# Optimization experiments

Hardware: AMD Instinct MI355X
Metric: run time of the kernel (lower is better)

Reference implementation:

```python
import jax, jax.numpy as jnp
import numpy as np

B, S, H, E = 4, 2048, 1024, 8

def setup_inputs() -> dict:
    key = jax.random.key(0)
    k1, k2, k3 = jax.random.split(key, 3)
    scale_g = 1.0 / np.sqrt(H)
    scale_e = 1.0 / np.sqrt(H)
    return {
        "x": jax.random.normal(k1, (B, S, H), dtype=jnp.float32),
        "gate_w": jax.random.normal(k2, (H, E), dtype=jnp.float32) * scale_g,
        "gate_b": jnp.zeros((E,), dtype=jnp.float32),
        "expert_w": jax.random.normal(k3, (E, H, H), dtype=jnp.float32) * scale_e,
        "expert_b": jnp.zeros((E, H), dtype=jnp.float32),
    }

def reference(x, gate_w, gate_b, expert_w, expert_b):
    b, s, h = x.shape
    tok = x.reshape(-1, h)                                  # [T, H]
    # gate: softmax over experts per token
    w = jax.nn.softmax(tok @ gate_w + gate_b, axis=-1)      # [T, E]
    # all experts applied to all tokens (dense MoE)
    eo = jnp.einsum("th,ehd->ted", tok, expert_w) + expert_b[None]  # [T, E, H]
    out = jnp.einsum("te,ted->td", w, eo)                   # [T, H]
    return out.reshape(b, s, h)
```

## Files before the change

kernel.cpp:

```cpp
#include <hip/hip_runtime.h>
#include <stdint.h>

typedef unsigned short u16;
typedef short bf8 __attribute__((ext_vector_type(8)));
typedef float f4 __attribute__((ext_vector_type(4)));

#define TTOK 8192
#define HD   1024
#define NE   8

static __device__ __forceinline__ u16 f2bf(float f) {
  union { float f; uint32_t u; } v; v.f = f;
  return (u16)((v.u + 0x7fffu + ((v.u >> 16) & 1u)) >> 16);
}

__global__ __launch_bounds__(256) void gate_conv_kernel(
    const float* __restrict__ x, const float* __restrict__ gw,
    const float* __restrict__ gb, float* __restrict__ wout,
    u16* __restrict__ abf)
{
  const int t    = blockIdx.x * 4 + (threadIdx.x >> 6);
  const int lane = threadIdx.x & 63;
  const float* xr = x + (size_t)t * HD;
  float p[NE];
#pragma unroll
  for (int e = 0; e < NE; ++e) p[e] = 0.f;
#pragma unroll 4
  for (int h = lane; h < HD; h += 64) {
    const float xv = xr[h];
    abf[(size_t)t * HD + h] = f2bf(xv);
    const float* g = gw + (size_t)h * NE;
#pragma unroll
    for (int e = 0; e < NE; ++e) p[e] += xv * g[e];
  }
#pragma unroll
  for (int e = 0; e < NE; ++e) {
#pragma unroll
    for (int off = 32; off > 0; off >>= 1)
      p[e] += __shfl_xor(p[e], off, 64);
    p[e] += gb[e];
  }
  float m = p[0];
#pragma unroll
  for (int e = 1; e < NE; ++e) m = fmaxf(m, p[e]);
  float s = 0.f;
#pragma unroll
  for (int e = 0; e < NE; ++e) { p[e] = expf(p[e] - m); s += p[e]; }
  const float inv = 1.f / s;
  if (lane == 0) {
#pragma unroll
    for (int e = 0; e < NE; ++e) wout[t * NE + e] = p[e] * inv;
  }
}

__global__ __launch_bounds__(256) void wconv_kernel(
    const float* __restrict__ ew, u16* __restrict__ wt)
{
  __shared__ u16 tile[64][66];
  const int e  = blockIdx.z;
  const int h0 = blockIdx.y * 64;
  const int d0 = blockIdx.x * 64;
  const int c  = threadIdx.x & 63;
  const int r0 = threadIdx.x >> 6;
  const float* src = ew + (size_t)e * HD * HD;
  u16* dst = wt + (size_t)e * HD * HD;
#pragma unroll
  for (int i = 0; i < 16; ++i) {
    const int r = i * 4 + r0;
    tile[r][c] = f2bf(src[(size_t)(h0 + r) * HD + d0 + c]);
  }
  __syncthreads();
#pragma unroll
  for (int i = 0; i < 16; ++i) {
    const int r = i * 4 + r0;
    dst[(size_t)(d0 + r) * HD + h0 + c] = tile[c][r];
  }
}

#define BM 128
#define BN 128
#define BK 64

#define MM(a_, b_, c_) __builtin_amdgcn_mfma_f32_16x16x32_bf16((a_), (b_), (c_), 0, 0, 0)

#define LDFA(off_, m_, kk_) (*(const bf8*)((const char*)As + (off_) + \
    (size_t)(wrb + (m_) * 16 + l15) * 128 + ((((kk_) * 4 + lhi) ^ (l15 & 7)) << 4)))
#define LDFB(off_, n_, kk_) (*(const bf8*)((const char*)Bs + (off_) + \
    (size_t)(wcb + (n_) * 16 + l15) * 128 + ((((kk_) * 4 + lhi) ^ (l15 & 7)) << 4)))

#define GL(srcp_, dstp_) __builtin_amdgcn_global_load_lds( \
    (const __attribute__((address_space(1))) void*)(srcp_), \
    (__attribute__((address_space(3))) void*)(dstp_), 16, 0, 0)

#define STAGE_A(sq_)                                                \
  {                                                                 \
    const int sk_ = ((sq_) & 15) << 6;                              \
    const u16* as_ = aSrc0 + sk_;                                   \
    char* ad_ = (char*)As + stO + tid * 16;                         \
    GL(as_,          ad_);                                          \
    GL(as_ + 32768,  ad_ +  4096);                                  \
    GL(as_ + 65536,  ad_ +  8192);                                  \
    GL(as_ + 98304,  ad_ + 12288);                                  \
  }
#define STAGE_B(sq_)                                                \
  {                                                                 \
    const int se_ = (sq_) >> 4;                                     \
    const int sk_ = ((sq_) & 15) << 6;                              \
    const u16* bs_ = bSrc0 + (size_t)se_ * (HD * HD) + sk_;         \
    char* bd_ = (char*)Bs + stO + tid * 16;                         \
    GL(bs_,          bd_);                                          \
    GL(bs_ + 32768,  bd_ +  4096);                                  \
    GL(bs_ + 65536,  bd_ +  8192);                                  \
    GL(bs_ + 98304,  bd_ + 12288);                                  \
  }

#define MFMA16                                            \
    acc[0][0] = MM(a0, b0, acc[0][0]);                    \
    acc[1][0] = MM(a1, b0, acc[1][0]);                    \
    acc[2][0] = MM(a2, b0, acc[2][0]);                    \
    acc[3][0] = MM(a3, b0, acc[3][0]);                    \
    acc[0][1] = MM(a0, b1, acc[0][1]);                    \
    acc[1][1] = MM(a1, b1, acc[1][1]);                    \
    acc[2][1] = MM(a2, b1, acc[2][1]);                    \
    acc[3][1] = MM(a3, b1, acc[3][1]);                    \
    acc[0][2] = MM(a0, b2, acc[0][2]);                    \
    acc[1][2] = MM(a1, b2, acc[1][2]);                    \
    acc[2][2] = MM(a2, b2, acc[2][2]);                    \
    acc[3][2] = MM(a3, b2, acc[3][2]);                    \
    acc[0][3] = MM(a0, b3, acc[0][3]);                    \
    acc[1][3] = MM(a1, b3, acc[1][3]);                    \
    acc[2][3] = MM(a2, b3, acc[2][3]);                    \
    acc[3][3] = MM(a3, b3, acc[3][3]);

#define READS(kk_)                                        \
    bf8 a0 = LDFA(curO, 0, kk_);                          \
    bf8 a1 = LDFA(curO, 1, kk_);                          \
    bf8 a2 = LDFA(curO, 2, kk_);                          \
    bf8 a3 = LDFA(curO, 3, kk_);                          \
    bf8 b0 = LDFB(curO, 0, kk_);                          \
    bf8 b1 = LDFB(curO, 1, kk_);                          \
    bf8 b2 = LDFB(curO, 2, kk_);                          \
    bf8 b3 = LDFB(curO, 3, kk_);

#define FOLD(e_)                                                      \
  {                                                                   \
    _Pragma("unroll")                                                 \
    for (int mi = 0; mi < 4; ++mi) {                                  \
      const int r_ = wrb + mi * 16 + lhi * 4;                         \
      const float w0 = wgs[(r_ + 0) * 9 + (e_)];                      \
      const float w1 = wgs[(r_ + 1) * 9 + (e_)];                      \
      const float w2 = wgs[(r_ + 2) * 9 + (e_)];                      \
      const float w3 = wgs[(r_ + 3) * 9 + (e_)];                      \
      _Pragma("unroll")                                               \
      for (int ni = 0; ni < 4; ++ni) {                                \
        accO[mi][ni][0] += w0 * acc[mi][ni][0];                       \
        accO[mi][ni][1] += w1 * acc[mi][ni][1];                       \
        accO[mi][ni][2] += w2 * acc[mi][ni][2];                       \
        accO[mi][ni][3] += w3 * acc[mi][ni][3];                       \
        acc[mi][ni] = fz;                                             \
      }                                                               \
    }                                                                 \
  }

#define BAR       __builtin_amdgcn_s_barrier();
#define LGKM0     asm volatile("s_waitcnt lgkmcnt(0)" ::: "memory");
#define VM0       asm volatile("s_waitcnt vmcnt(0)" ::: "memory");
#define PRIO1     __builtin_amdgcn_s_setprio(1);
#define PRIO0     __builtin_amdgcn_s_setprio(0);

__global__ __launch_bounds__(256, 2) void moe_gemm_kernel(
    const u16* __restrict__ A,
    const u16* __restrict__ Wt,
    const float* __restrict__ wg,
    const float* __restrict__ eb,
    float* __restrict__ out)
{
  __shared__ u16 As[2 * BM * BK];
  __shared__ u16 Bs[2 * BN * BK];
  __shared__ float wgs[BM * 9];

  const int bid   = blockIdx.x;
  const int xcd   = bid & 7;
  const int local = bid >> 3;
  const int bm    = xcd * 8 + (local & 7);
  const int bn    = local >> 3;
  const int row0  = bm * BM;
  const int col0  = bn * BN;

  const int tid  = threadIdx.x;
  const int lane = tid & 63;
  const int wid  = tid >> 6;
  const int wr   = wid >> 1;
  const int wc   = wid & 1;
  const int l15  = lane & 15;
  const int lhi  = lane >> 4;
  const int wrb  = wr * 64;
  const int wcb  = wc * 64;

  const int row_in = tid >> 3;
  const int gsw    = (tid & 7) ^ (row_in & 7);
  const u16* aSrc0 = A  + (size_t)(row0 + row_in) * HD + gsw * 8;
  const u16* bSrc0 = Wt + (size_t)(col0 + row_in) * HD + gsw * 8;

  {
    const f4 v = *(const f4*)(wg + (size_t)row0 * NE + tid * 4);
    const int i0 = tid * 4;
#pragma unroll
    for (int j = 0; j < 4; ++j) {
      const int idx = i0 + j;
      wgs[(idx >> 3) * 9 + (idx & 7)] = v[j];
    }
  }
  LGKM0

  const f4 fz = {0.f, 0.f, 0.f, 0.f};
  f4 acc[4][4], accO[4][4];
#pragma unroll
  for (int i = 0; i < 4; ++i)
#pragma unroll
    for (int j = 0; j < 4; ++j) { acc[i][j] = fz; accO[i][j] = fz; }

  int curO = 0, stO = 16384;

  { const int svO = stO; stO = 0; STAGE_A(0) STAGE_B(0) stO = svO; }

  for (int q = 0; q < 127; ++q) {
    VM0
    BAR
    {
      READS(0)
      STAGE_A(q + 1)
      BAR LGKM0 PRIO1
      MFMA16
      PRIO0 BAR
    }
    {
      READS(1)
      STAGE_B(q + 1)
      BAR LGKM0 PRIO1
      MFMA16
      PRIO0
    }
    { const int t_ = curO; curO = stO; stO = t_; }
    if ((q & 15) == 15) FOLD(q >> 4)
  }
  VM0
  BAR
  { READS(0) BAR LGKM0 PRIO1 MFMA16 PRIO0 BAR }
  { READS(1) BAR LGKM0 PRIO1 MFMA16 PRIO0 }
  FOLD(7)

  float ebv[4][8];
#pragma unroll
  for (int ni = 0; ni < 4; ++ni) {
    const int d = col0 + wcb + ni * 16 + l15;
#pragma unroll
    for (int e2 = 0; e2 < NE; ++e2) ebv[ni][e2] = eb[(size_t)e2 * HD + d];
  }
#pragma unroll
  for (int mi = 0; mi < 4; ++mi) {
    const int r_ = wrb + mi * 16 + lhi * 4;
#pragma unroll
    for (int j = 0; j < 4; ++j) {
      const int t = row0 + r_ + j;
      const float* wrow = &wgs[(r_ + j) * 9];
#pragma unroll
      for (int ni = 0; ni < 4; ++ni) {
        const float bias =
            wrow[0] * ebv[ni][0] + wrow[1] * ebv[ni][1] +
            wrow[2] * ebv[ni][2] + wrow[3] * ebv[ni][3] +
            wrow[4] * ebv[ni][4] + wrow[5] * ebv[ni][5] +
            wrow[6] * ebv[ni][6] + wrow[7] * ebv[ni][7];
        const int d = col0 + wcb + ni * 16 + l15;
        out[(size_t)t * HD + d] = accO[mi][ni][j] + bias;
      }
    }
  }
}

extern "C" void kernel_launch(void* const* d_in, const int* in_sizes, int n_in,
                              void* d_out, int out_size, void* d_ws, size_t ws_size,
                              hipStream_t stream) {
  const float* x  = (const float*)d_in[0];
  const float* gw = (const float*)d_in[1];
  const float* gb = (const float*)d_in[2];
  const float* ew = (const float*)d_in[3];
  const float* eb = (const float*)d_in[4];
  float* out = (float*)d_out;

  char* ws = (char*)d_ws;
  u16*   abf   = (u16*)ws;
  u16*   wt    = (u16*)(ws + (size_t)16 * 1024 * 1024);
  float* wgate = (float*)(ws + (size_t)32 * 1024 * 1024);

  gate_conv_kernel<<<dim3(TTOK / 4), dim3(256), 0, stream>>>(x, gw, gb, wgate, abf);
  wconv_kernel<<<dim3(16, 16, 8), dim3(256), 0, stream>>>(ew, wt);
  moe_gemm_kernel<<<dim3((TTOK / BM) * (HD / BN)), dim3(256), 0, stream>>>(abf, wt, wgate, eb, out);
}
```

Measured before the change: 164.4 us.

## Fold gate weights into A tile, split experts across blocks, add combine pass

Scales each A row by its gate weight while staging it into LDS, so the per-expert FOLD step goes away and one accumulator set covers all experts in a block. The grid becomes 256 blocks of 512 threads with 256x256 tiles, and each block handles half of the experts. The second half writes a bf16 partial that a new combine kernel adds into the output. In exchange it adds register-path A loads with conversion work, an extra kernel launch and extra global traffic, and rounds the partial to bf16, which costs precision.

```diff
diff --git a/kernel.cpp b/kernel.cpp
--- a/kernel.cpp
+++ b/kernel.cpp
@@ -4,6 +4,8 @@
 typedef unsigned short u16;
 typedef short bf8 __attribute__((ext_vector_type(8)));
 typedef float f4 __attribute__((ext_vector_type(4)));
+typedef unsigned int u32x4 __attribute__((ext_vector_type(4)));
+typedef short s8v __attribute__((ext_vector_type(8)));
 
 #define TTOK 8192
 #define HD   1024
@@ -12,6 +14,16 @@
 static __device__ __forceinline__ u16 f2bf(float f) {
   union { float f; uint32_t u; } v; v.f = f;
   return (u16)((v.u + 0x7fffu + ((v.u >> 16) & 1u)) >> 16);
+}
+
+static __device__ __forceinline__ uint32_t scale2bf(uint32_t v, float w) {
+  union { float f; uint32_t u; } lo, hi;
+  lo.u = v << 16;
+  hi.u = v & 0xffff0000u;
+  lo.f *= w; hi.f *= w;
+  const uint32_t lr = (lo.u + 0x7fffu + ((lo.u >> 16) & 1u)) >> 16;
+  const uint32_t hr = (hi.u + 0x7fffu + ((hi.u >> 16) & 1u)) & 0xffff0000u;
+  return lr | hr;
 }
 
 __global__ __launch_bounds__(256) void gate_conv_kernel(
@@ -77,8 +89,8 @@
   }
 }
 
-#define BM 128
-#define BN 128
+#define BM 256
+#define BN 256
 #define BK 64
 
 #define MM(a_, b_, c_) __builtin_amdgcn_mfma_f32_16x16x32_bf16((a_), (b_), (c_), 0, 0, 0)
@@ -92,190 +104,260 @@
     (const __attribute__((address_space(1))) void*)(srcp_), \
     (__attribute__((address_space(3))) void*)(dstp_), 16, 0, 0)
 
-#define STAGE_A(sq_)                                                \
-  {                                                                 \
-    const int sk_ = ((sq_) & 15) << 6;                              \
-    const u16* as_ = aSrc0 + sk_;                                   \
-    char* ad_ = (char*)As + stO + tid * 16;                         \
-    GL(as_,          ad_);                                          \
-    GL(as_ + 32768,  ad_ +  4096);                                  \
-    GL(as_ + 65536,  ad_ +  8192);                                  \
-    GL(as_ + 98304,  ad_ + 12288);                                  \
-  }
-#define STAGE_B(sq_)                                                \
-  {                                                                 \
-    const int se_ = (sq_) >> 4;                                     \
-    const int sk_ = ((sq_) & 15) << 6;                              \
-    const u16* bs_ = bSrc0 + (size_t)se_ * (HD * HD) + sk_;         \
-    char* bd_ = (char*)Bs + stO + tid * 16;                         \
-    GL(bs_,          bd_);                                          \
-    GL(bs_ + 32768,  bd_ +  4096);                                  \
-    GL(bs_ + 65536,  bd_ +  8192);                                  \
-    GL(bs_ + 98304,  bd_ + 12288);                                  \
-  }
-
-#define MFMA16                                            \
-    acc[0][0] = MM(a0, b0, acc[0][0]);                    \
-    acc[1][0] = MM(a1, b0, acc[1][0]);                    \
-    acc[2][0] = MM(a2, b0, acc[2][0]);                    \
-    acc[3][0] = MM(a3, b0, acc[3][0]);                    \
-    acc[0][1] = MM(a0, b1, acc[0][1]);                    \
-    acc[1][1] = MM(a1, b1, acc[1][1]);                    \
-    acc[2][1] = MM(a2, b1, acc[2][1]);                    \
-    acc[3][1] = MM(a3, b1, acc[3][1]);                    \
-    acc[0][2] = MM(a0, b2, acc[0][2]);                    \
-    acc[1][2] = MM(a1, b2, acc[1][2]);                    \
-    acc[2][2] = MM(a2, b2, acc[2][2]);                    \
-    acc[3][2] = MM(a3, b2, acc[3][2]);                    \
-    acc[0][3] = MM(a0, b3, acc[0][3]);                    \
-    acc[1][3] = MM(a1, b3, acc[1][3]);                    \
-    acc[2][3] = MM(a2, b3, acc[2][3]);                    \
-    acc[3][3] = MM(a3, b3, acc[3][3]);
-
-#define READS(kk_)                                        \
-    bf8 a0 = LDFA(curO, 0, kk_);                          \
-    bf8 a1 = LDFA(curO, 1, kk_);                          \
-    bf8 a2 = LDFA(curO, 2, kk_);                          \
-    bf8 a3 = LDFA(curO, 3, kk_);                          \
-    bf8 b0 = LDFB(curO, 0, kk_);                          \
-    bf8 b1 = LDFB(curO, 1, kk_);                          \
-    bf8 b2 = LDFB(curO, 2, kk_);                          \
-    bf8 b3 = LDFB(curO, 3, kk_);
-
-#define FOLD(e_)                                                      \
-  {                                                                   \
-    _Pragma("unroll")                                                 \
-    for (int mi = 0; mi < 4; ++mi) {                                  \
-      const int r_ = wrb + mi * 16 + lhi * 4;                         \
-      const float w0 = wgs[(r_ + 0) * 9 + (e_)];                      \
-      const float w1 = wgs[(r_ + 1) * 9 + (e_)];                      \
-      const float w2 = wgs[(r_ + 2) * 9 + (e_)];                      \
-      const float w3 = wgs[(r_ + 3) * 9 + (e_)];                      \
-      _Pragma("unroll")                                               \
-      for (int ni = 0; ni < 4; ++ni) {                                \
-        accO[mi][ni][0] += w0 * acc[mi][ni][0];                       \
-        accO[mi][ni][1] += w1 * acc[mi][ni][1];                       \
-        accO[mi][ni][2] += w2 * acc[mi][ni][2];                       \
-        accO[mi][ni][3] += w3 * acc[mi][ni][3];                       \
-        acc[mi][ni] = fz;                                             \
-      }                                                               \
-    }                                                                 \
+#define MFMA16(M_)                                        \
+    acc[(M_)+0][0] = MM(a0, b0, acc[(M_)+0][0]);          \
+    acc[(M_)+1][0] = MM(a1, b0, acc[(M_)+1][0]);          \
+    acc[(M_)+2][0] = MM(a2, b0, acc[(M_)+2][0]);          \
+    acc[(M_)+3][0] = MM(a3, b0, acc[(M_)+3][0]);          \
+    acc[(M_)+0][1] = MM(a0, b1, acc[(M_)+0][1]);          \
+    acc[(M_)+1][1] = MM(a1, b1, acc[(M_)+1][1]);          \
+    acc[(M_)+2][1] = MM(a2, b1, acc[(M_)+2][1]);          \
+    acc[(M_)+3][1] = MM(a3, b1, acc[(M_)+3][1]);          \
+    acc[(M_)+0][2] = MM(a0, b2, acc[(M_)+0][2]);          \
+    acc[(M_)+1][2] = MM(a1, b2, acc[(M_)+1][2]);          \
+    acc[(M_)+2][2] = MM(a2, b2, acc[(M_)+2][2]);          \
+    acc[(M_)+3][2] = MM(a3, b2, acc[(M_)+3][2]);          \
+    acc[(M_)+0][3] = MM(a0, b3, acc[(M_)+0][3]);          \
+    acc[(M_)+1][3] = MM(a1, b3, acc[(M_)+1][3]);          \
+    acc[(M_)+2][3] = MM(a2, b3, acc[(M_)+2][3]);          \
+    acc[(M_)+3][3] = MM(a3, b3, acc[(M_)+3][3]);
+
+#define RD_A(m0_, kk_)                                    \
+    a0 = LDFA(curO, (m0_)+0, kk_);                        \
+    a1 = LDFA(curO, (m0_)+1, kk_);                        \
+    a2 = LDFA(curO, (m0_)+2, kk_);                        \
+    a3 = LDFA(curO, (m0_)+3, kk_);
+#define RD_B(kk_)                                         \
+    b0 = LDFB(curO, 0, kk_);                              \
+    b1 = LDFB(curO, 1, kk_);                              \
+    b2 = LDFB(curO, 2, kk_);                              \
+    b3 = LDFB(curO, 3, kk_);
+
+#define A_WRITE(aL_, wA_, off_)  {                                   \
+    u32x4 t_;                                                        \
+    t_[0] = scale2bf((aL_)[0], wA_);                                 \
+    t_[1] = scale2bf((aL_)[1], wA_);                                 \
+    t_[2] = scale2bf((aL_)[2], wA_);                                 \
+    t_[3] = scale2bf((aL_)[3], wA_);                                 \
+    *(u32x4*)((char*)As + stO + awoff + (off_)) = t_;                \
   }
 
 #define BAR       __builtin_amdgcn_s_barrier();
 #define LGKM0     asm volatile("s_waitcnt lgkmcnt(0)" ::: "memory");
 #define VM0       asm volatile("s_waitcnt vmcnt(0)" ::: "memory");
+#define VMC4      asm volatile("s_waitcnt vmcnt(4)" ::: "memory");
 #define PRIO1     __builtin_amdgcn_s_setprio(1);
 #define PRIO0     __builtin_amdgcn_s_setprio(0);
 
-__global__ __launch_bounds__(256, 2) void moe_gemm_kernel(
+__global__ __launch_bounds__(512, 2) void moe_gemm_kernel(
     const u16* __restrict__ A,
     const u16* __restrict__ Wt,
     const float* __restrict__ wg,
     const float* __restrict__ eb,
-    float* __restrict__ out)
+    float* __restrict__ out,
+    u16* __restrict__ p1)
 {
   __shared__ u16 As[2 * BM * BK];
   __shared__ u16 Bs[2 * BN * BK];
   __shared__ float wgs[BM * 9];
 
-  const int bid   = blockIdx.x;
-  const int xcd   = bid & 7;
-  const int local = bid >> 3;
-  const int bm    = xcd * 8 + (local & 7);
-  const int bn    = local >> 3;
+  const int bid  = blockIdx.x;
+  const int xcd  = bid & 7;
+  const int j    = bid >> 3;
+  const int bm   = xcd * 4 + (j & 3);
+  const int r2   = j >> 2;
+  const int bn   = r2 & 3;
+  const int half = r2 >> 2;
+  const int eBase = half * 4;
   const int row0  = bm * BM;
   const int col0  = bn * BN;
 
   const int tid  = threadIdx.x;
   const int lane = tid & 63;
   const int wid  = tid >> 6;
-  const int wr   = wid >> 1;
-  const int wc   = wid & 1;
+  const int wr   = wid >> 2;
+  const int wc   = wid & 3;
   const int l15  = lane & 15;
   const int lhi  = lane >> 4;
-  const int wrb  = wr * 64;
+  const int wrb  = wr * 128;
   const int wcb  = wc * 64;
 
   const int row_in = tid >> 3;
   const int gsw    = (tid & 7) ^ (row_in & 7);
-  const u16* aSrc0 = A  + (size_t)(row0 + row_in) * HD + gsw * 8;
+  const int awoff  = row_in * 128 + gsw * 16;
+  const u16* aSrc0 = A  + (size_t)(row0 + row_in) * HD + (tid & 7) * 8;
   const u16* bSrc0 = Wt + (size_t)(col0 + row_in) * HD + gsw * 8;
 
   {
     const f4 v = *(const f4*)(wg + (size_t)row0 * NE + tid * 4);
     const int i0 = tid * 4;
 #pragma unroll
-    for (int j = 0; j < 4; ++j) {
-      const int idx = i0 + j;
-      wgs[(idx >> 3) * 9 + (idx & 7)] = v[j];
+    for (int k = 0; k < 4; ++k) {
+      const int idx = i0 + k;
+      wgs[(idx >> 3) * 9 + (idx & 7)] = v[k];
     }
   }
   LGKM0
+  BAR
+
+  float wA0 = wgs[(row_in +   0) * 9 + eBase];
+  float wA1 = wgs[(row_in +  64) * 9 + eBase];
+  float wA2 = wgs[(row_in + 128) * 9 + eBase];
+  float wA3 = wgs[(row_in + 192) * 9 + eBase];
+  size_t esHH = (size_t)eBase * (HD * HD);
 
   const f4 fz = {0.f, 0.f, 0.f, 0.f};
-  f4 acc[4][4], accO[4][4];
-#pragma unroll
-  for (int i = 0; i < 4; ++i)
-#pragma unroll
-    for (int j = 0; j < 4; ++j) { acc[i][j] = fz; accO[i][j] = fz; }
-
-  int curO = 0, stO = 16384;
-
-  { const int svO = stO; stO = 0; STAGE_A(0) STAGE_B(0) stO = svO; }
-
-  for (int q = 0; q < 127; ++q) {
-    VM0
-    BAR
+  f4 acc[8][4];
+#pragma unroll
+  for (int i = 0; i < 8; ++i)
+#pragma unroll
+    for (int k = 0; k < 4; ++k) acc[i][k] = fz;
+
+  int curO = 0, stO = 32768;
+  u32x4 aL0, aL1, aL2, aL3;
+  bf8 a0, a1, a2, a3, b0, b1, b2, b3;
+
+  {
+    aL0 = *(const u32x4*)(aSrc0);
+    aL1 = *(const u32x4*)(aSrc0 + 65536);
+    aL2 = *(const u32x4*)(aSrc0 + 131072);
+    aL3 = *(const u32x4*)(aSrc0 + 196608);
+    const u16* bS_ = bSrc0 + esHH;
+    char* bd_ = (char*)Bs + tid * 16;
+    GL(bS_, bd_); GL(bS_ + 65536, bd_ + 8192);
+    GL(bS_ + 131072, bd_ + 16384); GL(bS_ + 196608, bd_ + 24576);
+    VMC4
+    { const int svO = stO; stO = 0;
+      A_WRITE(aL0, wA0, 0) A_WRITE(aL1, wA1, 8192)
+      A_WRITE(aL2, wA2, 16384) A_WRITE(aL3, wA3, 24576)
+      stO = svO; }
+    VM0 LGKM0 BAR
+  }
+
+  for (int q = 0; q < 63; ++q) {
+    const int sq    = q + 1;
+    const int kcol_ = (sq & 15) << 6;
+    if ((sq & 15) == 0) {
+      const int es_ = eBase + (sq >> 4);
+      esHH = (size_t)es_ * (HD * HD);
+      wA0 = wgs[(row_in +   0) * 9 + es_];
+      wA1 = wgs[(row_in +  64) * 9 + es_];
+      wA2 = wgs[(row_in + 128) * 9 + es_];
+      wA3 = wgs[(row_in + 192) * 9 + es_];
+    }
+    RD_A(0, 0) RD_B(0)
     {
-      READS(0)
-      STAGE_A(q + 1)
-      BAR LGKM0 PRIO1
-      MFMA16
-      PRIO0 BAR
-    }
+      const u16* aS_ = aSrc0 + kcol_;
+      aL0 = *(const u32x4*)(aS_);
+      aL1 = *(const u32x4*)(aS_ + 65536);
+      aL2 = *(const u32x4*)(aS_ + 131072);
+      aL3 = *(const u32x4*)(aS_ + 196608);
+    }
+    BAR LGKM0 PRIO1
+    MFMA16(0)
+    PRIO0 BAR
+    RD_A(4, 0)
     {
-      READS(1)
-      STAGE_B(q + 1)
-      BAR LGKM0 PRIO1
-      MFMA16
-      PRIO0
-    }
+      const u16* bS_ = bSrc0 + esHH + kcol_;
+      char* bd_ = (char*)Bs + stO + tid * 16;
+      GL(bS_, bd_); GL(bS_ + 65536, bd_ + 8192);
+      GL(bS_ + 131072, bd_ + 16384); GL(bS_ + 196608, bd_ + 24576);
+    }
+    BAR LGKM0 PRIO1
+    MFMA16(4)
+    PRIO0 BAR
+    RD_A(0, 1) RD_B(1)
+    VMC4
+    A_WRITE(aL0, wA0, 0) A_WRITE(aL1, wA1, 8192)
+    A_WRITE(aL2, wA2, 16384) A_WRITE(aL3, wA3, 24576)
+    BAR LGKM0 PRIO1
+    MFMA16(0)
+    PRIO0 BAR
+    RD_A(4, 1)
+    BAR LGKM0 PRIO1
+    MFMA16(4)
+    PRIO0
+    VM0 BAR
     { const int t_ = curO; curO = stO; stO = t_; }
-    if ((q & 15) == 15) FOLD(q >> 4)
-  }
-  VM0
-  BAR
-  { READS(0) BAR LGKM0 PRIO1 MFMA16 PRIO0 BAR }
-  { READS(1) BAR LGKM0 PRIO1 MFMA16 PRIO0 }
-  FOLD(7)
-
-  float ebv[4][8];
-#pragma unroll
-  for (int ni = 0; ni < 4; ++ni) {
-    const int d = col0 + wcb + ni * 16 + l15;
-#pragma unroll
-    for (int e2 = 0; e2 < NE; ++e2) ebv[ni][e2] = eb[(size_t)e2 * HD + d];
-  }
-#pragma unroll
-  for (int mi = 0; mi < 4; ++mi) {
-    const int r_ = wrb + mi * 16 + lhi * 4;
-#pragma unroll
-    for (int j = 0; j < 4; ++j) {
-      const int t = row0 + r_ + j;
-      const float* wrow = &wgs[(r_ + j) * 9];
-#pragma unroll
-      for (int ni = 0; ni < 4; ++ni) {
-        const float bias =
-            wrow[0] * ebv[ni][0] + wrow[1] * ebv[ni][1] +
-            wrow[2] * ebv[ni][2] + wrow[3] * ebv[ni][3] +
-            wrow[4] * ebv[ni][4] + wrow[5] * ebv[ni][5] +
-            wrow[6] * ebv[ni][6] + wrow[7] * ebv[ni][7];
-        const int d = col0 + wcb + ni * 16 + l15;
-        out[(size_t)t * HD + d] = accO[mi][ni][j] + bias;
+  }
+  RD_A(0, 0) RD_B(0)
+  BAR LGKM0 PRIO1
+  MFMA16(0)
+  PRIO0 BAR
+  RD_A(4, 0)
+  BAR LGKM0 PRIO1
+  MFMA16(4)
+  PRIO0 BAR
+  RD_A(0, 1) RD_B(1)
+  BAR LGKM0 PRIO1
+  MFMA16(0)
+  PRIO0 BAR
+  RD_A(4, 1)
+  BAR LGKM0 PRIO1
+  MFMA16(4)
+  PRIO0
+
+  if (half == 0) {
+    float ebv[4][8];
+#pragma unroll
+    for (int ni = 0; ni < 4; ++ni) {
+      const int d = col0 + wcb + ni * 16 + l15;
+#pragma unroll
+      for (int e2 = 0; e2 < NE; ++e2) ebv[ni][e2] = eb[(size_t)e2 * HD + d];
+    }
+#pragma unroll
+    for (int mi = 0; mi < 8; ++mi) {
+      const int r_ = wrb + mi * 16 + lhi * 4;
+#pragma unroll
+      for (int jj = 0; jj < 4; ++jj) {
+        const int t = row0 + r_ + jj;
+        const float* wrow = &wgs[(r_ + jj) * 9];
+#pragma unroll
+        for (int ni = 0; ni < 4; ++ni) {
+          const float bias =
+              wrow[0] * ebv[ni][0] + wrow[1] * ebv[ni][1] +
+              wrow[2] * ebv[ni][2] + wrow[3] * ebv[ni][3] +
+              wrow[4] * ebv[ni][4] + wrow[5] * ebv[ni][5] +
+              wrow[6] * ebv[ni][6] + wrow[7] * ebv[ni][7];
+          const int d = col0 + wcb + ni * 16 + l15;
+          out[(size_t)t * HD + d] = acc[mi][ni][jj] + bias;
+        }
       }
     }
-  }
+  } else {
+#pragma unroll
+    for (int mi = 0; mi < 8; ++mi) {
+      const int r_ = wrb + mi * 16 + lhi * 4;
+#pragma unroll
+      for (int jj = 0; jj < 4; ++jj) {
+        const int t = row0 + r_ + jj;
+#pragma unroll
+        for (int ni = 0; ni < 4; ++ni) {
+          const int d = col0 + wcb + ni * 16 + l15;
+          p1[(size_t)t * HD + d] = f2bf(acc[mi][ni][jj]);
+        }
+      }
+    }
+  }
+}
+
+__global__ __launch_bounds__(256) void combine_kernel(
+    float* __restrict__ out, const u16* __restrict__ p1)
+{
+  const size_t i8 = ((size_t)blockIdx.x * 256 + threadIdx.x) * 8;
+  f4 o0 = *(f4*)(out + i8);
+  f4 o1 = *(f4*)(out + i8 + 4);
+  const s8v pv = *(const s8v*)(p1 + i8);
+#pragma unroll
+  for (int k = 0; k < 4; ++k) {
+    union { uint32_t u; float f; } c0, c1;
+    c0.u = ((uint32_t)(u16)pv[k]) << 16;
+    c1.u = ((uint32_t)(u16)pv[k + 4]) << 16;
+    o0[k] += c0.f;
+    o1[k] += c1.f;
+  }
+  *(f4*)(out + i8) = o0;
+  *(f4*)(out + i8 + 4) = o1;
 }
 
 extern "C" void kernel_launch(void* const* d_in, const int* in_sizes, int n_in,
@@ -292,8 +374,10 @@
   u16*   abf   = (u16*)ws;
   u16*   wt    = (u16*)(ws + (size_t)16 * 1024 * 1024);
   float* wgate = (float*)(ws + (size_t)32 * 1024 * 1024);
+  u16*   p1    = (u16*)(ws + (size_t)34 * 1024 * 1024);
 
   gate_conv_kernel<<<dim3(TTOK / 4), dim3(256), 0, stream>>>(x, gw, gb, wgate, abf);
   wconv_kernel<<<dim3(16, 16, 8), dim3(256), 0, stream>>>(ew, wt);
-  moe_gemm_kernel<<<dim3((TTOK / BM) * (HD / BN)), dim3(256), 0, stream>>>(abf, wt, wgate, eb, out);
-}
+  moe_gemm_kernel<<<dim3(256), dim3(512), 0, stream>>>(abf, wt, wgate, eb, out, p1);
+  combine_kernel<<<dim3(TTOK * HD / (256 * 8)), dim3(256), 0, stream>>>(out, p1);
+}
```

After: 188.7 us. +14.7%, slower.

## Process two experts per K-pass with 256-row tiles and fp16 output accumulators

Applied to the files above, without the earlier changes.

Grows the block tile to 256 rows and 512 threads. Each k-step now stages B tiles for two experts at once, so every A fragment is reused across two experts' MFMAs and the K loop runs half as many iterations. The weighted per-expert fold goes into packed fp16 accumulators to save registers for the doubled fp32 MFMA accumulators. This cuts how often A must be restaged, but fp16 accumulation of the output loses precision and may breach tolerance. The larger shared-memory footprint and register use also risk lower occupancy.

```diff
diff --git a/kernel.cpp b/kernel.cpp
--- a/kernel.cpp
+++ b/kernel.cpp
@@ -4,10 +4,12 @@
 typedef unsigned short u16;
 typedef short bf8 __attribute__((ext_vector_type(8)));
 typedef float f4 __attribute__((ext_vector_type(4)));
+typedef _Float16 h2 __attribute__((ext_vector_type(2)));
 
 #define TTOK 8192
 #define HD   1024
 #define NE   8
+#define HH   (HD * HD)
 
 static __device__ __forceinline__ u16 f2bf(float f) {
   union { float f; uint32_t u; } v; v.f = f;
@@ -62,8 +64,8 @@
   const int d0 = blockIdx.x * 64;
   const int c  = threadIdx.x & 63;
   const int r0 = threadIdx.x >> 6;
-  const float* src = ew + (size_t)e * HD * HD;
-  u16* dst = wt + (size_t)e * HD * HD;
+  const float* src = ew + (size_t)e * HH;
+  u16* dst = wt + (size_t)e * HH;
 #pragma unroll
   for (int i = 0; i < 16; ++i) {
     const int r = i * 4 + r0;
@@ -77,16 +79,12 @@
   }
 }
 
-#define BM 128
+#define BM 256
 #define BN 128
 #define BK 64
+#define SLOT 65536
 
 #define MM(a_, b_, c_) __builtin_amdgcn_mfma_f32_16x16x32_bf16((a_), (b_), (c_), 0, 0, 0)
-
-#define LDFA(off_, m_, kk_) (*(const bf8*)((const char*)As + (off_) + \
-    (size_t)(wrb + (m_) * 16 + l15) * 128 + ((((kk_) * 4 + lhi) ^ (l15 & 7)) << 4)))
-#define LDFB(off_, n_, kk_) (*(const bf8*)((const char*)Bs + (off_) + \
-    (size_t)(wcb + (n_) * 16 + l15) * 128 + ((((kk_) * 4 + lhi) ^ (l15 & 7)) << 4)))
 
 #define GL(srcp_, dstp_) __builtin_amdgcn_global_load_lds( \
     (const __attribute__((address_space(1))) void*)(srcp_), \
@@ -96,70 +94,96 @@
   {                                                                 \
     const int sk_ = ((sq_) & 15) << 6;                              \
     const u16* as_ = aSrc0 + sk_;                                   \
-    char* ad_ = (char*)As + stO + tid * 16;                         \
+    char* ad_ = smem + stS + tid * 16;                              \
     GL(as_,          ad_);                                          \
-    GL(as_ + 32768,  ad_ +  4096);                                  \
-    GL(as_ + 65536,  ad_ +  8192);                                  \
-    GL(as_ + 98304,  ad_ + 12288);                                  \
+    GL(as_ +  65536, ad_ +  8192);                                  \
+    GL(as_ + 131072, ad_ + 16384);                                  \
+    GL(as_ + 196608, ad_ + 24576);                                  \
   }
 #define STAGE_B(sq_)                                                \
   {                                                                 \
-    const int se_ = (sq_) >> 4;                                     \
+    const int pn_ = (sq_) >> 4;                                     \
     const int sk_ = ((sq_) & 15) << 6;                              \
-    const u16* bs_ = bSrc0 + (size_t)se_ * (HD * HD) + sk_;         \
-    char* bd_ = (char*)Bs + stO + tid * 16;                         \
-    GL(bs_,          bd_);                                          \
-    GL(bs_ + 32768,  bd_ +  4096);                                  \
-    GL(bs_ + 65536,  bd_ +  8192);                                  \
-    GL(bs_ + 98304,  bd_ + 12288);                                  \
-  }
-
-#define MFMA16                                            \
-    acc[0][0] = MM(a0, b0, acc[0][0]);                    \
-    acc[1][0] = MM(a1, b0, acc[1][0]);                    \
-    acc[2][0] = MM(a2, b0, acc[2][0]);                    \
-    acc[3][0] = MM(a3, b0, acc[3][0]);                    \
-    acc[0][1] = MM(a0, b1, acc[0][1]);                    \
-    acc[1][1] = MM(a1, b1, acc[1][1]);                    \
-    acc[2][1] = MM(a2, b1, acc[2][1]);                    \
-    acc[3][1] = MM(a3, b1, acc[3][1]);                    \
-    acc[0][2] = MM(a0, b2, acc[0][2]);                    \
-    acc[1][2] = MM(a1, b2, acc[1][2]);                    \
-    acc[2][2] = MM(a2, b2, acc[2][2]);                    \
-    acc[3][2] = MM(a3, b2, acc[3][2]);                    \
-    acc[0][3] = MM(a0, b3, acc[0][3]);                    \
-    acc[1][3] = MM(a1, b3, acc[1][3]);                    \
-    acc[2][3] = MM(a2, b3, acc[2][3]);                    \
-    acc[3][3] = MM(a3, b3, acc[3][3]);
-
-#define READS(kk_)                                        \
-    bf8 a0 = LDFA(curO, 0, kk_);                          \
-    bf8 a1 = LDFA(curO, 1, kk_);                          \
-    bf8 a2 = LDFA(curO, 2, kk_);                          \
-    bf8 a3 = LDFA(curO, 3, kk_);                          \
-    bf8 b0 = LDFB(curO, 0, kk_);                          \
-    bf8 b1 = LDFB(curO, 1, kk_);                          \
-    bf8 b2 = LDFB(curO, 2, kk_);                          \
-    bf8 b3 = LDFB(curO, 3, kk_);
-
-#define FOLD(e_)                                                      \
-  {                                                                   \
-    _Pragma("unroll")                                                 \
-    for (int mi = 0; mi < 4; ++mi) {                                  \
-      const int r_ = wrb + mi * 16 + lhi * 4;                         \
-      const float w0 = wgs[(r_ + 0) * 9 + (e_)];                      \
-      const float w1 = wgs[(r_ + 1) * 9 + (e_)];                      \
-      const float w2 = wgs[(r_ + 2) * 9 + (e_)];                      \
-      const float w3 = wgs[(r_ + 3) * 9 + (e_)];                      \
-      _Pragma("unroll")                                               \
-      for (int ni = 0; ni < 4; ++ni) {                                \
-        accO[mi][ni][0] += w0 * acc[mi][ni][0];                       \
-        accO[mi][ni][1] += w1 * acc[mi][ni][1];                       \
-        accO[mi][ni][2] += w2 * acc[mi][ni][2];                       \
-        accO[mi][ni][3] += w3 * acc[mi][ni][3];                       \
-        acc[mi][ni] = fz;                                             \
-      }                                                               \
-    }                                                                 \
+    const u16* b0_ = bSrc0 + (size_t)(2 * pn_) * HH + sk_;          \
+    char* bd_ = smem + stS + 32768 + tid * 16;                      \
+    GL(b0_,          bd_);                                          \
+    GL(b0_ +  65536, bd_ +  8192);                                  \
+    GL(b0_ + HH,          bd_ + 16384);                             \
+    GL(b0_ + HH + 65536,  bd_ + 24576);                             \
+  }
+
+#define READS(aP_, bP_)                                   \
+    bf8 a0  = *(const bf8*)(aP_);                         \
+    bf8 a1  = *(const bf8*)((aP_) + 2048);                \
+    bf8 a2  = *(const bf8*)((aP_) + 4096);                \
+    bf8 a3  = *(const bf8*)((aP_) + 6144);                \
+    bf8 b00 = *(const bf8*)(bP_);                         \
+    bf8 b01 = *(const bf8*)((bP_) + 2048);                \
+    bf8 b02 = *(const bf8*)((bP_) + 4096);                \
+    bf8 b03 = *(const bf8*)((bP_) + 6144);                \
+    bf8 b10 = *(const bf8*)((bP_) + 16384);               \
+    bf8 b11 = *(const bf8*)((bP_) + 18432);               \
+    bf8 b12 = *(const bf8*)((bP_) + 20480);               \
+    bf8 b13 = *(const bf8*)((bP_) + 22528);
+
+#define MFMA32                                            \
+    acc0[0][0] = MM(a0, b00, acc0[0][0]);                 \
+    acc0[1][0] = MM(a1, b00, acc0[1][0]);                 \
+    acc0[2][0] = MM(a2, b00, acc0[2][0]);                 \
+    acc0[3][0] = MM(a3, b00, acc0[3][0]);                 \
+    acc0[0][1] = MM(a0, b01, acc0[0][1]);                 \
+    acc0[1][1] = MM(a1, b01, acc0[1][1]);                 \
+    acc0[2][1] = MM(a2, b01, acc0[2][1]);                 \
+    acc0[3][1] = MM(a3, b01, acc0[3][1]);                 \
+    acc0[0][2] = MM(a0, b02, acc0[0][2]);                 \
+    acc0[1][2] = MM(a1, b02, acc0[1][2]);                 \
+    acc0[2][2] = MM(a2, b02, acc0[2][2]);                 \
+    acc0[3][2] = MM(a3, b02, acc0[3][2]);                 \
+    acc0[0][3] = MM(a0, b03, acc0[0][3]);                 \
+    acc0[1][3] = MM(a1, b03, acc0[1][3]);                 \
+    acc0[2][3] = MM(a2, b03, acc0[2][3]);                 \
+    acc0[3][3] = MM(a3, b03, acc0[3][3]);                 \
+    acc1[0][0] = MM(a0, b10, acc1[0][0]);                 \
+    acc1[1][0] = MM(a1, b10, acc1[1][0]);                 \
+    acc1[2][0] = MM(a2, b10, acc1[2][0]);                 \
+    acc1[3][0] = MM(a3, b10, acc1[3][0]);                 \
+    acc1[0][1] = MM(a0, b11, acc1[0][1]);                 \
+    acc1[1][1] = MM(a1, b11, acc1[1][1]);                 \
+    acc1[2][1] = MM(a2, b11, acc1[2][1]);                 \
+    acc1[3][1] = MM(a3, b11, acc1[3][1]);                 \
+    acc1[0][2] = MM(a0, b12, acc1[0][2]);                 \
+    acc1[1][2] = MM(a1, b12, acc1[1][2]);                 \
+    acc1[2][2] = MM(a2, b12, acc1[2][2]);                 \
+    acc1[3][2] = MM(a3, b12, acc1[3][2]);                 \
+    acc1[0][3] = MM(a0, b13, acc1[0][3]);                 \
+    acc1[1][3] = MM(a1, b13, acc1[1][3]);                 \
+    acc1[2][3] = MM(a2, b13, acc1[2][3]);                 \
+    acc1[3][3] = MM(a3, b13, acc1[3][3]);
+
+#define FOLD(e0_, e1_)                                                  \
+  {                                                                     \
+    _Pragma("unroll")                                                   \
+    for (int mi = 0; mi < 4; ++mi) {                                    \
+      const int r_ = wrb + mi * 16 + lhi * 4;                           \
+      float wa[4], wb[4];                                               \
+      _Pragma("unroll")                                                 \
+      for (int j = 0; j < 4; ++j) {                                     \
+        wa[j] = wgs[(r_ + j) * 9 + (e0_)];                              \
+        wb[j] = wgs[(r_ + j) * 9 + (e1_)];                              \
+      }                                                                 \
+      _Pragma("unroll")                                                 \
+      for (int ni = 0; ni < 4; ++ni) {                                  \
+        const float f0 = wa[0] * acc0[mi][ni][0] + wb[0] * acc1[mi][ni][0]; \
+        const float f1 = wa[1] * acc0[mi][ni][1] + wb[1] * acc1[mi][ni][1]; \
+        const float f2 = wa[2] * acc0[mi][ni][2] + wb[2] * acc1[mi][ni][2]; \
+        const float f3 = wa[3] * acc0[mi][ni][3] + wb[3] * acc1[mi][ni][3]; \
+        h2 t0; t0[0] = (_Float16)f0; t0[1] = (_Float16)f1;              \
+        h2 t1; t1[0] = (_Float16)f2; t1[1] = (_Float16)f3;              \
+        accP0[mi][ni] += t0;                                            \
+        accP1[mi][ni] += t1;                                            \
+        acc0[mi][ni] = fz; acc1[mi][ni] = fz;                           \
+      }                                                                 \
+    }                                                                   \
   }
 
 #define BAR       __builtin_amdgcn_s_barrier();
@@ -168,22 +192,21 @@
 #define PRIO1     __builtin_amdgcn_s_setprio(1);
 #define PRIO0     __builtin_amdgcn_s_setprio(0);
 
-__global__ __launch_bounds__(256, 2) void moe_gemm_kernel(
+__global__ __launch_bounds__(512, 2) void moe_gemm_kernel(
     const u16* __restrict__ A,
     const u16* __restrict__ Wt,
     const float* __restrict__ wg,
     const float* __restrict__ eb,
     float* __restrict__ out)
 {
-  __shared__ u16 As[2 * BM * BK];
-  __shared__ u16 Bs[2 * BN * BK];
-  __shared__ float wgs[BM * 9];
+  __shared__ __attribute__((aligned(16))) char smem[2 * SLOT + 9216];
+  float* wgs = (float*)(smem + 2 * SLOT);
 
   const int bid   = blockIdx.x;
   const int xcd   = bid & 7;
   const int local = bid >> 3;
-  const int bm    = xcd * 8 + (local & 7);
-  const int bn    = local >> 3;
+  const int bm    = xcd * 4 + (local & 3);
+  const int bn    = local >> 2;
   const int row0  = bm * BM;
   const int col0  = bn * BN;
 
@@ -197,6 +220,12 @@
   const int wrb  = wr * 64;
   const int wcb  = wc * 64;
 
+  const int gsl   = (lhi ^ (l15 & 7)) << 4;
+  const int thrA0 = wrb * 128 + l15 * 128 + gsl;
+  const int thrA1 = thrA0 ^ 64;
+  const int thrB0 = 32768 + wcb * 128 + l15 * 128 + gsl;
+  const int thrB1 = thrB0 ^ 64;
+
   const int row_in = tid >> 3;
   const int gsw    = (tid & 7) ^ (row_in & 7);
   const u16* aSrc0 = A  + (size_t)(row0 + row_in) * HD + gsw * 8;
@@ -206,49 +235,64 @@
     const f4 v = *(const f4*)(wg + (size_t)row0 * NE + tid * 4);
     const int i0 = tid * 4;
 #pragma unroll
+    for (int k = 0; k < 4; ++k) {
+      const int idx = i0 + k;
+      wgs[(idx >> 3) * 9 + (idx & 7)] = v[k];
+    }
+  }
+  LGKM0
+
+  const f4 fz = {0.f, 0.f, 0.f, 0.f};
+  const h2 hz = {(_Float16)0.f, (_Float16)0.f};
+  f4 acc0[4][4], acc1[4][4];
+  h2 accP0[4][4], accP1[4][4];
+#pragma unroll
+  for (int i = 0; i < 4; ++i)
+#pragma unroll
     for (int j = 0; j < 4; ++j) {
-      const int idx = i0 + j;
-      wgs[(idx >> 3) * 9 + (idx & 7)] = v[j];
-    }
-  }
-  LGKM0
-
-  const f4 fz = {0.f, 0.f, 0.f, 0.f};
-  f4 acc[4][4], accO[4][4];
-#pragma unroll
-  for (int i = 0; i < 4; ++i)
-#pragma unroll
-    for (int j = 0; j < 4; ++j) { acc[i][j] = fz; accO[i][j] = fz; }
-
-  int curO = 0, stO = 16384;
-
-  { const int svO = stO; stO = 0; STAGE_A(0) STAGE_B(0) stO = svO; }
-
-  for (int q = 0; q < 127; ++q) {
+      acc0[i][j] = fz; acc1[i][j] = fz;
+      accP0[i][j] = hz; accP1[i][j] = hz;
+    }
+
+  int curS = 0, stS = SLOT;
+
+  { const int sv = stS; stS = 0; STAGE_A(0) STAGE_B(0) stS = sv; }
+
+  for (int q = 0; q < 63; ++q) {
     VM0
     BAR
+    const char* aP0 = smem + curS + thrA0;
+    const char* aP1 = smem + curS + thrA1;
+    const char* bP0 = smem + curS + thrB0;
+    const char* bP1 = smem + curS + thrB1;
     {
-      READS(0)
+      READS(aP0, bP0)
       STAGE_A(q + 1)
       BAR LGKM0 PRIO1
-      MFMA16
+      MFMA32
       PRIO0 BAR
     }
     {
-      READS(1)
+      READS(aP1, bP1)
       STAGE_B(q + 1)
       BAR LGKM0 PRIO1
-      MFMA16
+      MFMA32
       PRIO0
     }
-    { const int t_ = curO; curO = stO; stO = t_; }
-    if ((q & 15) == 15) FOLD(q >> 4)
+    { const int t_ = curS; curS = stS; stS = t_; }
+    if ((q & 15) == 15) { const int p_ = q >> 4; FOLD(2 * p_, 2 * p_ + 1) }
   }
   VM0
   BAR
-  { READS(0) BAR LGKM0 PRIO1 MFMA16 PRIO0 BAR }
-  { READS(1) BAR LGKM0 PRIO1 MFMA16 PRIO0 }
-  FOLD(7)
+  {
+    const char* aP0 = smem + curS + thrA0;
+    const char* aP1 = smem + curS + thrA1;
+    const char* bP0 = smem + curS + thrB0;
+    const char* bP1 = smem + curS + thrB1;
+    { READS(aP0, bP0) BAR LGKM0 PRIO1 MFMA32 PRIO0 BAR }
+    { READS(aP1, bP1) BAR LGKM0 PRIO1 MFMA32 PRIO0 }
+  }
+  FOLD(6, 7)
 
   float ebv[4][8];
 #pragma unroll
@@ -271,8 +315,10 @@
             wrow[2] * ebv[ni][2] + wrow[3] * ebv[ni][3] +
             wrow[4] * ebv[ni][4] + wrow[5] * ebv[ni][5] +
             wrow[6] * ebv[ni][6] + wrow[7] * ebv[ni][7];
+        const float v = (j < 2) ? (float)accP0[mi][ni][j & 1]
+                                : (float)accP1[mi][ni][j & 1];
         const int d = col0 + wcb + ni * 16 + l15;
-        out[(size_t)t * HD + d] = accO[mi][ni][j] + bias;
+        out[(size_t)t * HD + d] = v + bias;
       }
     }
   }
@@ -295,5 +341,5 @@
 
   gate_conv_kernel<<<dim3(TTOK / 4), dim3(256), 0, stream>>>(x, gw, gb, wgate, abf);
   wconv_kernel<<<dim3(16, 16, 8), dim3(256), 0, stream>>>(ew, wt);
-  moe_gemm_kernel<<<dim3((TTOK / BM) * (HD / BN)), dim3(256), 0, stream>>>(abf, wt, wgate, eb, out);
-}
+  moe_gemm_kernel<<<dim3((TTOK / BM) * (HD / BN)), dim3(512), 0, stream>>>(abf, wt, wgate, eb, out);
+}
```

Measured after the change: 140.2 us. 1.17x faster.
